# Kernel tuning notes

Measured on AMD Instinct MI355X. Metric: run time of the kernel, lower is better.

## Reference

```python
import jax, jax.numpy as jnp
import numpy as np

C = 128
NUM_GROUPS = 32
EPS = 1e-6


def setup_inputs() -> dict:
    key = jax.random.key(0)
    ks = jax.random.split(key, 6)
    B, H, W = 8, 64, 64
    x = jax.random.normal(ks[0], (B, C, H, W), dtype=jnp.float32)
    # 1x1 conv weights stored as [out_c, in_c] (kernel spatial dims are 1)
    fan_avg = C  # fan_in == fan_out == C for 1x1 conv
    bound = np.sqrt(3.0 / fan_avg)
    wq = jax.random.uniform(ks[1], (C, C), jnp.float32, -bound, bound)
    wk = jax.random.uniform(ks[2], (C, C), jnp.float32, -bound, bound)
    wv = jax.random.uniform(ks[3], (C, C), jnp.float32, -bound, bound)
    # proj_out has init_scale=0.0 -> near-zero init; use tiny random instead to test math
    wo = jax.random.uniform(ks[4], (C, C), jnp.float32, -bound, bound) * 1e-3
    bq = jnp.zeros((C,), jnp.float32)
    bk = jnp.zeros((C,), jnp.float32)
    bv = jnp.zeros((C,), jnp.float32)
    bo = jnp.zeros((C,), jnp.float32)
    gamma = jnp.ones((C,), jnp.float32)
    beta = jnp.zeros((C,), jnp.float32)
    return {"x": x, "gamma": gamma, "beta": beta,
            "wq": wq, "bq": bq, "wk": wk, "bk": bk,
            "wv": wv, "bv": bv, "wo": wo, "bo": bo}


def _group_norm(x, gamma, beta):
    B, Ch, H, W = x.shape
    g = NUM_GROUPS
    xg = x.reshape(B, g, Ch // g, H, W)
    mean = jnp.mean(xg, axis=(2, 3, 4), keepdims=True)
    var = jnp.var(xg, axis=(2, 3, 4), keepdims=True)
    xn = ((xg - mean) * jax.lax.rsqrt(var + EPS)).reshape(B, Ch, H, W)
    return xn * gamma[None, :, None, None] + beta[None, :, None, None]


def _conv1x1(x, w, b):
    # x: [B,C,H,W], w: [O,C], b: [O]
    return jnp.einsum('bchw,oc->bohw', x, w) + b[None, :, None, None]


def reference(x, gamma, beta, wq, bq, wk, bk, wv, bv, wo, bo):
    B, Ch, H, W = x.shape
    n = H * W
    h = _group_norm(x, gamma, beta)
    q = _conv1x1(h, wq, bq).reshape(B, Ch, n)
    k = _conv1x1(h, wk, bk).reshape(B, Ch, n)
    v = _conv1x1(h, wv, bv).reshape(B, Ch, n)
    # attn[b, i, j] = sum_c q[b,c,i] * k[b,c,j] / sqrt(C)
    attn = jnp.einsum('bci,bcj->bij', q, k) * (float(Ch) ** -0.5)
    attn = jax.nn.softmax(attn, axis=-1)
    # h[b,c,i] = sum_j v[b,c,j] * attn[b,i,j]
    out = jnp.einsum('bcj,bij->bci', v, attn).reshape(B, Ch, H, W)
    out = _conv1x1(out, wo, bo)
    return x + out
```

## Files before the change

### kernel.cpp

```cpp
#include <hip/hip_runtime.h>


typedef float f32x4 __attribute__((ext_vector_type(4)));
typedef short short8 __attribute__((ext_vector_type(8)));
typedef _Float16 half8 __attribute__((ext_vector_type(8)));
typedef _Float16 half2t __attribute__((ext_vector_type(2)));
typedef unsigned short ush;
typedef unsigned short ush4 __attribute__((ext_vector_type(4)));

__device__ __forceinline__ ush f2bf(float f) {
  unsigned u = __builtin_bit_cast(unsigned, f);
  u = (u + 0x7FFFu + ((u >> 16) & 1u)) >> 16;
  return (ush)u;
}
__device__ __forceinline__ float bf2f(ush v) {
  unsigned u = ((unsigned)v) << 16;
  return __builtin_bit_cast(float, u);
}
__device__ __forceinline__ unsigned f2fp8(float x) {
  unsigned u = __builtin_bit_cast(unsigned, x);
  unsigned s = (u >> 24) & 0x80u;
  unsigned au = u & 0x7fffffffu;
  if (au < 0x3A800000u) return s;
  if (au >= 0x43E00000u) return s | 0x7Eu;
  int e = (int)(au >> 23) - 127;
  if (e < -6) {
    float a = __builtin_bit_cast(float, au);
    int m = (int)(a * 512.0f + 0.5f);
    if (m >= 8) return s | 0x08u;
    return s | (unsigned)m;
  }
  unsigned keep = au >> 20, rem = au & 0xFFFFFu;
  keep += (rem > 0x80000u) || ((rem == 0x80000u) && (keep & 1u));
  int ef = (int)(keep >> 3) - 127;
  if (ef >= 8 && ((ef > 8) || ((keep & 7u) == 7u))) return s | 0x7Eu;
  return s | (unsigned)(((ef + 7) << 3) | (int)(keep & 7u));
}
__device__ __forceinline__ void async16(const void* g, void* l) {
  __builtin_amdgcn_global_load_lds(
      (const __attribute__((address_space(1))) unsigned int*)g,
      (__attribute__((address_space(3))) unsigned int*)l, 16, 0, 0);
}

__global__ __launch_bounds__(256) void gn_stats_kernel(
    const float* __restrict__ x, const float* __restrict__ gamma,
    const float* __restrict__ beta, const float* __restrict__ wo,
    float* __restrict__ scale_c, float* __restrict__ shift_c,
    ush* __restrict__ wob) {
  int bg = blockIdx.x;
  int b = bg >> 5, g = bg & 31;
  int tid = threadIdx.x;
  if (bg < 16) {
    int v4 = (bg * 256 + tid) * 4;
    float4 w4 = *(const float4*)(wo + v4);
    ush4 pk;
    pk.x = f2bf(w4.x); pk.y = f2bf(w4.y);
    pk.z = f2bf(w4.z); pk.w = f2bf(w4.w);
    *(ush4*)(wob + v4) = pk;
  }
  const float4* base = (const float4*)(x + (size_t)bg * 16384);
  float s = 0.f, sq = 0.f;
#pragma unroll
  for (int p = 0; p < 16; ++p) {
    float4 v = base[p * 256 + tid];
    s += (v.x + v.y) + (v.z + v.w);
    sq += (v.x * v.x + v.y * v.y) + (v.z * v.z + v.w * v.w);
  }
#pragma unroll
  for (int off = 32; off > 0; off >>= 1) {
    s += __shfl_down(s, off);
    sq += __shfl_down(sq, off);
  }
  __shared__ float rs[4], rq[4], mv[2];
  int w = tid >> 6, lane = tid & 63;
  if (lane == 0) { rs[w] = s; rq[w] = sq; }
  __syncthreads();
  if (tid == 0) {
    float S = (rs[0] + rs[1]) + (rs[2] + rs[3]);
    float Q = (rq[0] + rq[1]) + (rq[2] + rq[3]);
    float mean = S * (1.f / 16384.f);
    float var = Q * (1.f / 16384.f) - mean * mean;
    mv[0] = mean;
    mv[1] = rsqrtf(var + 1e-6f);
  }
  __syncthreads();
  if (tid < 4) {
    int c = (g << 2) + tid;
    float sc = mv[1] * gamma[c];
    scale_c[(b << 7) + c] = sc;
    shift_c[(b << 7) + c] = beta[c] - mv[0] * sc;
  }
}

__global__ __launch_bounds__(256) void qkv_kernel(
    const float* __restrict__ x, const float* __restrict__ scale_c,
    const float* __restrict__ shift_c, const float* __restrict__ wq,
    const float* __restrict__ wk, const float* __restrict__ wv,
    const float* __restrict__ bq, const float* __restrict__ bk,
    const float* __restrict__ bv, char* __restrict__ Qt8,
    char* __restrict__ Kt8, _Float16* __restrict__ Vh) {
  __shared__ __align__(16) ush hs[64 * 136];
  __shared__ __align__(16) ush wol[128 * 136];
  char* hs8 = (char*)hs;
  int bx = blockIdx.x;
  int type = bx >> 9;
  int rb = bx & 511;
  int b = rb >> 6, i0 = (rb & 63) << 6;
  int tid = threadIdx.x;
  int w = tid >> 6, lane = tid & 63, ln15 = lane & 15, quad = lane >> 4;

#pragma unroll
  for (int p = 0; p < 8; ++p) {
    int id = p * 256 + tid;
    int i = id & 63;
    int g8 = id >> 6;
    int c0 = g8 << 2;
    const float* xp = x + (((size_t)((b << 7) + c0)) << 12) + i0 + i;
    ush4 pk4;
#pragma unroll
    for (int e = 0; e < 4; ++e) {
      float h = xp[(size_t)e << 12] * scale_c[(b << 7) + c0 + e] +
                shift_c[(b << 7) + c0 + e];
      pk4[e] = f2bf(h);
    }
    int pg = g8 ^ ((i & 15) << 1);
    *(ush4*)(hs8 + i * 272 + pg * 8) = pk4;
  }
  const float* W = type == 0 ? wq : (type == 1 ? wk : wv);
#pragma unroll
  for (int p = 0; p < 16; ++p) {
    int v = p * 256 + tid;
    int o = v >> 5, cv = (v & 31) << 2;
    float4 w4 = *(const float4*)(W + (o << 7) + cv);
    uint2 pk;
    pk.x = (unsigned)f2bf(w4.x) | ((unsigned)f2bf(w4.y) << 16);
    pk.y = (unsigned)f2bf(w4.z) | ((unsigned)f2bf(w4.w) << 16);
    *(uint2*)&wol[o * 136 + cv] = pk;
  }
  __syncthreads();

#define HS_FRAG(row, dc) \
  (*(const short8*)(hs8 + (row) * 272 + (((((dc)*4 + quad)) ^ ((row)&15)) << 4)))

  if (type < 2) {
    f32x4 acc[8] = {};
    int hrow = w * 16 + ln15;
#pragma unroll
    for (int dc = 0; dc < 4; ++dc) {
      short8 af = HS_FRAG(hrow, dc);
#pragma unroll
      for (int nb = 0; nb < 8; ++nb) {
        short8 bf = *(const short8*)&wol[(nb * 16 + ln15) * 136 + dc * 32 + quad * 8];
        acc[nb] = __builtin_amdgcn_mfma_f32_16x16x32_bf16(af, bf, acc[nb], 0, 0, 0);
      }
    }
    const float* bias = type == 0 ? bq : bk;
    char* dst8 = type == 0 ? Qt8 : Kt8;
    __syncthreads();
#pragma unroll
    for (int nb = 0; nb < 8; ++nb) {
      int o = nb * 16 + ln15;
      float bi = bias[o];
#pragma unroll
      for (int r = 0; r < 4; ++r) {
        float val = acc[nb][r] + bi;
        if (type == 0) val *= 0.12751742f;
        hs8[(w * 16 + quad * 4 + r) * 144 + o] = (char)f2fp8(val);
      }
    }
    __syncthreads();
    int i = tid >> 2, seg = tid & 3;
    uint4 d0 = *(const uint4*)(hs8 + i * 144 + seg * 32);
    uint4 d1 = *(const uint4*)(hs8 + i * 144 + seg * 32 + 16);
    char* drow = dst8 + (((size_t)((b << 12) + i0 + i)) << 7) + seg * 32;
    *(uint4*)drow = d0;
    *(uint4*)(drow + 16) = d1;
  } else {
    f32x4 acc[8] = {};
    int hrow = w * 16 + ln15;
#pragma unroll
    for (int dc = 0; dc < 4; ++dc) {
      short8 bf = HS_FRAG(hrow, dc);
#pragma unroll
      for (int mb = 0; mb < 8; ++mb) {
        short8 af = *(const short8*)&wol[(mb * 16 + ln15) * 136 + dc * 32 + quad * 8];
        acc[mb] = __builtin_amdgcn_mfma_f32_16x16x32_bf16(af, bf, acc[mb], 0, 0, 0);
      }
    }
#pragma unroll
    for (int mb = 0; mb < 8; ++mb) {
#pragma unroll
      for (int r = 0; r < 4; ++r) {
        int o = mb * 16 + quad * 4 + r;
        float val = acc[mb][r] + bv[o];
        Vh[(((size_t)((b << 7) + o)) << 12) + i0 + w * 16 + ln15] = (_Float16)val;
      }
    }
  }
#undef HS_FRAG
}

__global__ __launch_bounds__(256, 3) void attn_kernel(
    const char* __restrict__ Qt8, const char* __restrict__ Kt8,
    const _Float16* __restrict__ Vh, ush* __restrict__ po,
    float* __restrict__ lw) {
  __shared__ __align__(16) char ksb[2][4096];
  __shared__ __align__(16) _Float16 vsb[2][4096];
  int bx = blockIdx.x;
  int b = bx & 7, qt = (bx >> 3) & 31, ksid = bx >> 8;
  int tid = threadIdx.x;
  int w = tid >> 6, lane = tid & 63, ln15 = lane & 15, quad = lane >> 4;
  int qbase = (qt << 7) + (w << 5);
  int j0 = ksid << 10;

  long qf[2][4];
#pragma unroll
  for (int ih = 0; ih < 2; ++ih) {
    const char* qrow =
        Qt8 + (((size_t)((b << 12) + qbase + ih * 16 + ln15)) << 7);
#pragma unroll
    for (int dc = 0; dc < 4; ++dc)
      qf[ih][dc] = *(const long*)(qrow + dc * 32 + quad * 8);
  }

  int kj = (w << 3) + (lane >> 3);
  int kh = (kj & 3) | (((kj >> 3) & 1) << 2);
  int kg = (lane & 7) ^ kh;
  const char* ksrc = Kt8 + (((size_t)((b << 12) + j0 + kj)) << 7) + (kg << 4);
  int d0r = (w << 5) + (lane >> 2);
  int d1r = d0r + 16;
  int vg0 = (lane & 3) ^ (((d0r >> 1) + (d0r >> 3)) & 3);
  int vg1 = (lane & 3) ^ (((d1r >> 1) + (d1r >> 3)) & 3);
  const _Float16* vsrc0 =
      Vh + (((size_t)((b << 7) + d0r)) << 12) + j0 + (vg0 << 3);
  const _Float16* vsrc1 =
      Vh + (((size_t)((b << 7) + d1r)) << 12) + j0 + (vg1 << 3);
  char* kdA = &ksb[0][0] + (w << 10);
  char* kdB = &ksb[1][0] + (w << 10);
  char* vdA0 = (char*)&vsb[0][0] + ((w * 2 + 0) << 10);
  char* vdA1 = (char*)&vsb[0][0] + ((w * 2 + 1) << 10);
  char* vdB0 = (char*)&vsb[1][0] + ((w * 2 + 0) << 10);
  char* vdB1 = (char*)&vsb[1][0] + ((w * 2 + 1) << 10);

  async16(ksrc, kdA);
  async16(vsrc0, vdA0);
  async16(vsrc1, vdA1);
  __syncthreads();

  f32x4 O[2][8] = {};
  float lsum[2] = {0.f, 0.f};
  const f32x4 SINIT = {-7.2134752f, -7.2134752f, -7.2134752f, -7.2134752f};
  int r0 = ((ln15 >> 2) << 3) + (ln15 & 3), r1 = r0 + 4;
  int hr = (ln15 & 3) | (((ln15 >> 2) & 1) << 2);

  for (int jt = 0; jt < 32; ++jt) {
    int buf = jt & 1;
    if (jt + 1 < 32) {
      ksrc += 4096;
      vsrc0 += 32;
      vsrc1 += 32;
      if (buf == 0) {
        async16(ksrc, kdB);
        async16(vsrc0, vdB0);
        async16(vsrc1, vdB1);
      } else {
        async16(ksrc, kdA);
        async16(vsrc0, vdA0);
        async16(vsrc1, vdA1);
      }
    }
    const char* kb = &ksb[buf][0];
    const char* vb = (const char*)&vsb[buf][0];

    f32x4 S[2][2];
#pragma unroll
    for (int ih = 0; ih < 2; ++ih) { S[ih][0] = SINIT; S[ih][1] = SINIT; }
#pragma unroll
    for (int dc = 0; dc < 4; ++dc) {
      int goff = ((((dc * 2 + (quad >> 1))) ^ hr) << 4) + ((quad & 1) << 3);
      long kf0 = *(const long*)(kb + r0 * 128 + goff);
      long kf1 = *(const long*)(kb + r1 * 128 + goff);
#pragma unroll
      for (int ih = 0; ih < 2; ++ih) {
        S[ih][0] = __builtin_amdgcn_mfma_f32_16x16x32_fp8_fp8(kf0, qf[ih][dc], S[ih][0], 0, 0, 0);
        S[ih][1] = __builtin_amdgcn_mfma_f32_16x16x32_fp8_fp8(kf1, qf[ih][dc], S[ih][1], 0, 0, 0);
      }
    }
    half8 pf[2];
#pragma unroll
    for (int ih = 0; ih < 2; ++ih) {
      float ls = 0.f;
      half8 p;
#pragma unroll
      for (int t = 0; t < 2; ++t) {
        float p0 = __builtin_amdgcn_exp2f(S[ih][t][0]);
        float p1 = __builtin_amdgcn_exp2f(S[ih][t][1]);
        float p2 = __builtin_amdgcn_exp2f(S[ih][t][2]);
        float p3 = __builtin_amdgcn_exp2f(S[ih][t][3]);
        ls += (p0 + p1) + (p2 + p3);
        half2t h01 = __builtin_bit_cast(half2t, __builtin_amdgcn_cvt_pkrtz(p0, p1));
        half2t h23 = __builtin_bit_cast(half2t, __builtin_amdgcn_cvt_pkrtz(p2, p3));
        p[t * 4 + 0] = h01.x; p[t * 4 + 1] = h01.y;
        p[t * 4 + 2] = h23.x; p[t * 4 + 3] = h23.y;
      }
      pf[ih] = p;
      lsum[ih] += ls;
    }
#pragma unroll
    for (int nb = 0; nb < 8; ++nb) {
      int d = nb * 16 + ln15;
      int sd = ((d >> 1) + (d >> 3)) & 3;
      half8 vf = *(const half8*)(vb + d * 64 + ((quad ^ sd) << 4));
#pragma unroll
      for (int ih = 0; ih < 2; ++ih)
        O[ih][nb] = __builtin_amdgcn_mfma_f32_16x16x32_f16(vf, pf[ih], O[ih][nb], 0, 0, 0);
    }
    __syncthreads();
  }

#pragma unroll
  for (int ih = 0; ih < 2; ++ih) {
    float l = lsum[ih];
    l += __shfl_xor(l, 16);
    l += __shfl_xor(l, 32);
    if (quad == 0) lw[(ksid << 15) + (b << 12) + qbase + ih * 16 + ln15] = l;
    int i = qbase + ih * 16 + ln15;
    size_t rowb = (((size_t)((ksid * 8 + b)) << 12) + i) << 7;
#pragma unroll
    for (int nb = 0; nb < 8; ++nb) {
      ush4 pk;
      pk.x = f2bf(O[ih][nb][0]);
      pk.y = f2bf(O[ih][nb][1]);
      pk.z = f2bf(O[ih][nb][2]);
      pk.w = f2bf(O[ih][nb][3]);
      *(ush4*)(po + rowb + nb * 16 + quad * 4) = pk;
    }
  }
}

__global__ __launch_bounds__(256) void proj_kernel(
    const float* __restrict__ x, const ush* __restrict__ po,
    const float* __restrict__ lw, const ush* __restrict__ wob,
    const float* __restrict__ bo, float* __restrict__ out) {
  int bx = blockIdx.x;
  int b = bx >> 6, i0 = (bx & 63) << 6;
  int tid = threadIdx.x;
  int w = tid >> 6, lane = tid & 63, ln15 = lane & 15, quad = lane >> 4;
  int i = i0 + w * 16 + ln15;
  float rl = 0.f;
#pragma unroll
  for (int s = 0; s < 4; ++s) rl += lw[(s << 15) + (b << 12) + i];
  float rinv = 1.f / rl;

  f32x4 acc[8] = {};
#pragma unroll
  for (int dc = 0; dc < 4; ++dc) {
    float vsum[8] = {0.f, 0.f, 0.f, 0.f, 0.f, 0.f, 0.f, 0.f};
#pragma unroll
    for (int s = 0; s < 4; ++s) {
      short8 pv = *(const short8*)(po + (((size_t)(s * 8 + b)) << 19) +
                                   ((size_t)i << 7) + dc * 32 + quad * 8);
#pragma unroll
      for (int e = 0; e < 8; ++e) vsum[e] += bf2f((ush)pv[e]);
    }
    short8 bfv;
#pragma unroll
    for (int e = 0; e < 8; ++e) bfv[e] = (short)f2bf(vsum[e] * rinv);
#pragma unroll
    for (int mb = 0; mb < 8; ++mb) {
      short8 af = *(const short8*)(wob + ((mb * 16 + ln15) << 7) + dc * 32 +
                                   quad * 8);
      acc[mb] = __builtin_amdgcn_mfma_f32_16x16x32_bf16(af, bfv, acc[mb], 0, 0, 0);
    }
  }
#pragma unroll
  for (int mb = 0; mb < 8; ++mb) {
#pragma unroll
    for (int r = 0; r < 4; ++r) {
      int o = mb * 16 + quad * 4 + r;
      size_t idx = (((size_t)(b << 7) + o) << 12) + i;
      out[idx] = x[idx] + acc[mb][r] + bo[o];
    }
  }
}

extern "C" void kernel_launch(void* const* d_in, const int* in_sizes, int n_in,
                              void* d_out, int out_size, void* d_ws,
                              size_t ws_size, hipStream_t stream) {
  const float* x = (const float*)d_in[0];
  const float* gamma = (const float*)d_in[1];
  const float* beta = (const float*)d_in[2];
  const float* wq = (const float*)d_in[3];
  const float* bq = (const float*)d_in[4];
  const float* wk = (const float*)d_in[5];
  const float* bk = (const float*)d_in[6];
  const float* wv = (const float*)d_in[7];
  const float* bv = (const float*)d_in[8];
  const float* wo = (const float*)d_in[9];
  const float* bo = (const float*)d_in[10];
  float* out = (float*)d_out;

  const size_t NE = (size_t)8 * 4096 * 128;
  char* Qt8 = (char*)d_ws;
  char* Kt8 = Qt8 + NE;
  _Float16* Vh = (_Float16*)(Kt8 + NE);
  ush* po = (ush*)(Vh + NE);
  float* lwp = (float*)(po + 4 * NE);
  float* scale_c = lwp + 4 * 32768;
  float* shift_c = scale_c + 1024;
  ush* wob = (ush*)(shift_c + 1024);

  gn_stats_kernel<<<256, 256, 0, stream>>>(x, gamma, beta, wo, scale_c,
                                           shift_c, wob);
  qkv_kernel<<<1536, 256, 0, stream>>>(x, scale_c, shift_c, wq, wk, wv, bq, bk,
                                       bv, Qt8, Kt8, Vh);
  attn_kernel<<<1024, 256, 0, stream>>>(Qt8, Kt8, Vh, po, lwp);
  proj_kernel<<<512, 256, 0, stream>>>(x, po, lwp, wob, bo, out);
}
```

Before: 200.0 us.

## Software-pipeline QK^T one tile ahead of softmax and PV in attention loop

Restructures the attention inner loop so the QK^T scores for tile jt+1 are computed while the exp/PV work for tile jt proceeds. K is now prefetched two tiles ahead and V one tile ahead in separate double buffers. Matrix phases are wrapped in s_setprio to raise wave priority during MFMA issue. The goal is to hide exp latency and LDS load latency behind matrix work, at the cost of more live registers (an extra score array) and an extra barrier in the prologue.

```diff
diff --git a/kernel.cpp b/kernel.cpp
--- a/kernel.cpp
+++ b/kernel.cpp
@@ -245,6 +245,8 @@
   async16(ksrc, kdA);
   async16(vsrc0, vdA0);
   async16(vsrc1, vdA1);
+  ksrc += 4096;
+  async16(ksrc, kdB);
   __syncthreads();
 
   f32x4 O[2][8] = {};
@@ -253,28 +255,11 @@
   int r0 = ((ln15 >> 2) << 3) + (ln15 & 3), r1 = r0 + 4;
   int hr = (ln15 & 3) | (((ln15 >> 2) & 1) << 2);
 
-  for (int jt = 0; jt < 32; ++jt) {
-    int buf = jt & 1;
-    if (jt + 1 < 32) {
-      ksrc += 4096;
-      vsrc0 += 32;
-      vsrc1 += 32;
-      if (buf == 0) {
-        async16(ksrc, kdB);
-        async16(vsrc0, vdB0);
-        async16(vsrc1, vdB1);
-      } else {
-        async16(ksrc, kdA);
-        async16(vsrc0, vdA0);
-        async16(vsrc1, vdA1);
-      }
-    }
-    const char* kb = &ksb[buf][0];
-    const char* vb = (const char*)&vsb[buf][0];
-
-    f32x4 S[2][2];
-#pragma unroll
-    for (int ih = 0; ih < 2; ++ih) { S[ih][0] = SINIT; S[ih][1] = SINIT; }
+  f32x4 Sc[2][2];
+#pragma unroll
+  for (int ih = 0; ih < 2; ++ih) { Sc[ih][0] = SINIT; Sc[ih][1] = SINIT; }
+  {
+    const char* kb = &ksb[0][0];
 #pragma unroll
     for (int dc = 0; dc < 4; ++dc) {
       int goff = ((((dc * 2 + (quad >> 1))) ^ hr) << 4) + ((quad & 1) << 3);
@@ -282,10 +267,51 @@
       long kf1 = *(const long*)(kb + r1 * 128 + goff);
 #pragma unroll
       for (int ih = 0; ih < 2; ++ih) {
-        S[ih][0] = __builtin_amdgcn_mfma_f32_16x16x32_fp8_fp8(kf0, qf[ih][dc], S[ih][0], 0, 0, 0);
-        S[ih][1] = __builtin_amdgcn_mfma_f32_16x16x32_fp8_fp8(kf1, qf[ih][dc], S[ih][1], 0, 0, 0);
-      }
-    }
+        Sc[ih][0] = __builtin_amdgcn_mfma_f32_16x16x32_fp8_fp8(kf0, qf[ih][dc], Sc[ih][0], 0, 0, 0);
+        Sc[ih][1] = __builtin_amdgcn_mfma_f32_16x16x32_fp8_fp8(kf1, qf[ih][dc], Sc[ih][1], 0, 0, 0);
+      }
+    }
+  }
+  __syncthreads();
+
+  for (int jt = 0; jt < 32; ++jt) {
+    if (jt + 2 < 32) {
+      ksrc += 4096;
+      async16(ksrc, (jt & 1) ? kdB : kdA);
+    }
+    if (jt + 1 < 32) {
+      vsrc0 += 32;
+      vsrc1 += 32;
+      if (jt & 1) {
+        async16(vsrc0, vdA0);
+        async16(vsrc1, vdA1);
+      } else {
+        async16(vsrc0, vdB0);
+        async16(vsrc1, vdB1);
+      }
+    }
+    const char* kbn = (jt & 1) ? &ksb[0][0] : &ksb[1][0];
+    const char* vb = (const char*)((jt & 1) ? &vsb[1][0] : &vsb[0][0]);
+
+    f32x4 Sn[2][2];
+    if (jt + 1 < 32) {
+#pragma unroll
+      for (int ih = 0; ih < 2; ++ih) { Sn[ih][0] = SINIT; Sn[ih][1] = SINIT; }
+      __builtin_amdgcn_s_setprio(1);
+#pragma unroll
+      for (int dc = 0; dc < 4; ++dc) {
+        int goff = ((((dc * 2 + (quad >> 1))) ^ hr) << 4) + ((quad & 1) << 3);
+        long kf0 = *(const long*)(kbn + r0 * 128 + goff);
+        long kf1 = *(const long*)(kbn + r1 * 128 + goff);
+#pragma unroll
+        for (int ih = 0; ih < 2; ++ih) {
+          Sn[ih][0] = __builtin_amdgcn_mfma_f32_16x16x32_fp8_fp8(kf0, qf[ih][dc], Sn[ih][0], 0, 0, 0);
+          Sn[ih][1] = __builtin_amdgcn_mfma_f32_16x16x32_fp8_fp8(kf1, qf[ih][dc], Sn[ih][1], 0, 0, 0);
+        }
+      }
+      __builtin_amdgcn_s_setprio(0);
+    }
+
     half8 pf[2];
 #pragma unroll
     for (int ih = 0; ih < 2; ++ih) {
@@ -293,10 +319,10 @@
       half8 p;
 #pragma unroll
       for (int t = 0; t < 2; ++t) {
-        float p0 = __builtin_amdgcn_exp2f(S[ih][t][0]);
-        float p1 = __builtin_amdgcn_exp2f(S[ih][t][1]);
-        float p2 = __builtin_amdgcn_exp2f(S[ih][t][2]);
-        float p3 = __builtin_amdgcn_exp2f(S[ih][t][3]);
+        float p0 = __builtin_amdgcn_exp2f(Sc[ih][t][0]);
+        float p1 = __builtin_amdgcn_exp2f(Sc[ih][t][1]);
+        float p2 = __builtin_amdgcn_exp2f(Sc[ih][t][2]);
+        float p3 = __builtin_amdgcn_exp2f(Sc[ih][t][3]);
         ls += (p0 + p1) + (p2 + p3);
         half2t h01 = __builtin_bit_cast(half2t, __builtin_amdgcn_cvt_pkrtz(p0, p1));
         half2t h23 = __builtin_bit_cast(half2t, __builtin_amdgcn_cvt_pkrtz(p2, p3));
@@ -306,6 +332,8 @@
       pf[ih] = p;
       lsum[ih] += ls;
     }
+
+    __builtin_amdgcn_s_setprio(1);
 #pragma unroll
     for (int nb = 0; nb < 8; ++nb) {
       int d = nb * 16 + ln15;
@@ -315,7 +343,16 @@
       for (int ih = 0; ih < 2; ++ih)
         O[ih][nb] = __builtin_amdgcn_mfma_f32_16x16x32_f16(vf, pf[ih], O[ih][nb], 0, 0, 0);
     }
+    __builtin_amdgcn_s_setprio(0);
     __syncthreads();
+
+    if (jt + 1 < 32) {
+#pragma unroll
+      for (int ih = 0; ih < 2; ++ih) {
+        Sc[ih][0] = Sn[ih][0];
+        Sc[ih][1] = Sn[ih][1];
+      }
+    }
   }
 
 #pragma unroll
```

Result: no change. 199.4 us (-0.3%).

## Use 4-stage LDS ring with prefetch distance two and explicit vmcnt waits

Applied to the files above, without the earlier changes.

The attention kernel's K/V shared-memory staging changes from a double buffer to a four-slot ring. Loads are issued two tiles ahead, and each iteration waits on vmcnt with a single barrier instead of the trailing __syncthreads. It also raises wave priority around the MFMA blocks with s_setprio. This should hide global-to-LDS latency better, but it doubles LDS use (48KB per block), which may limit occupancy under launch_bounds(256,3).

```diff
diff --git a/kernel.cpp b/kernel.cpp
--- a/kernel.cpp
+++ b/kernel.cpp
@@ -204,8 +204,8 @@
     const char* __restrict__ Qt8, const char* __restrict__ Kt8,
     const _Float16* __restrict__ Vh, ush* __restrict__ po,
     float* __restrict__ lw) {
-  __shared__ __align__(16) char ksb[2][4096];
-  __shared__ __align__(16) _Float16 vsb[2][4096];
+  __shared__ __align__(16) char ksb[4][4096];
+  __shared__ __align__(16) _Float16 vsb[4][4096];
   int bx = blockIdx.x;
   int b = bx & 7, qt = (bx >> 3) & 31, ksid = bx >> 8;
   int tid = threadIdx.x;
@@ -235,17 +235,18 @@
       Vh + (((size_t)((b << 7) + d0r)) << 12) + j0 + (vg0 << 3);
   const _Float16* vsrc1 =
       Vh + (((size_t)((b << 7) + d1r)) << 12) + j0 + (vg1 << 3);
-  char* kdA = &ksb[0][0] + (w << 10);
-  char* kdB = &ksb[1][0] + (w << 10);
-  char* vdA0 = (char*)&vsb[0][0] + ((w * 2 + 0) << 10);
-  char* vdA1 = (char*)&vsb[0][0] + ((w * 2 + 1) << 10);
-  char* vdB0 = (char*)&vsb[1][0] + ((w * 2 + 0) << 10);
-  char* vdB1 = (char*)&vsb[1][0] + ((w * 2 + 1) << 10);
-
-  async16(ksrc, kdA);
-  async16(vsrc0, vdA0);
-  async16(vsrc1, vdA1);
-  __syncthreads();
+
+  asm volatile("s_waitcnt vmcnt(0)" ::: "memory");
+
+  async16(ksrc, &ksb[0][0] + (w << 10));
+  async16(vsrc0, (char*)&vsb[0][0] + ((2 * w + 0) << 10));
+  async16(vsrc1, (char*)&vsb[0][0] + ((2 * w + 1) << 10));
+  ksrc += 4096;
+  vsrc0 += 32;
+  vsrc1 += 32;
+  async16(ksrc, &ksb[1][0] + (w << 10));
+  async16(vsrc0, (char*)&vsb[1][0] + ((2 * w + 0) << 10));
+  async16(vsrc1, (char*)&vsb[1][0] + ((2 * w + 1) << 10));
 
   f32x4 O[2][8] = {};
   float lsum[2] = {0.f, 0.f};
@@ -254,27 +255,28 @@
   int hr = (ln15 & 3) | (((ln15 >> 2) & 1) << 2);
 
   for (int jt = 0; jt < 32; ++jt) {
-    int buf = jt & 1;
-    if (jt + 1 < 32) {
+    if (jt < 31)
+      asm volatile("s_waitcnt vmcnt(3)" ::: "memory");
+    else
+      asm volatile("s_waitcnt vmcnt(0)" ::: "memory");
+    __builtin_amdgcn_s_barrier();
+
+    if (jt + 2 < 32) {
       ksrc += 4096;
       vsrc0 += 32;
       vsrc1 += 32;
-      if (buf == 0) {
-        async16(ksrc, kdB);
-        async16(vsrc0, vdB0);
-        async16(vsrc1, vdB1);
-      } else {
-        async16(ksrc, kdA);
-        async16(vsrc0, vdA0);
-        async16(vsrc1, vdA1);
-      }
-    }
-    const char* kb = &ksb[buf][0];
-    const char* vb = (const char*)&vsb[buf][0];
+      int rd = (jt + 2) & 3;
+      async16(ksrc, &ksb[rd][0] + (w << 10));
+      async16(vsrc0, (char*)&vsb[rd][0] + ((2 * w + 0) << 10));
+      async16(vsrc1, (char*)&vsb[rd][0] + ((2 * w + 1) << 10));
+    }
+    const char* kb = &ksb[jt & 3][0];
+    const char* vb = (const char*)&vsb[jt & 3][0];
 
     f32x4 S[2][2];
 #pragma unroll
     for (int ih = 0; ih < 2; ++ih) { S[ih][0] = SINIT; S[ih][1] = SINIT; }
+    __builtin_amdgcn_s_setprio(1);
 #pragma unroll
     for (int dc = 0; dc < 4; ++dc) {
       int goff = ((((dc * 2 + (quad >> 1))) ^ hr) << 4) + ((quad & 1) << 3);
@@ -286,6 +288,8 @@
         S[ih][1] = __builtin_amdgcn_mfma_f32_16x16x32_fp8_fp8(kf1, qf[ih][dc], S[ih][1], 0, 0, 0);
       }
     }
+    __builtin_amdgcn_s_setprio(0);
+
     half8 pf[2];
 #pragma unroll
     for (int ih = 0; ih < 2; ++ih) {
@@ -306,6 +310,8 @@
       pf[ih] = p;
       lsum[ih] += ls;
     }
+
+    __builtin_amdgcn_s_setprio(1);
 #pragma unroll
     for (int nb = 0; nb < 8; ++nb) {
       int d = nb * 16 + ln15;
@@ -315,7 +321,7 @@
       for (int ih = 0; ih < 2; ++ih)
         O[ih][nb] = __builtin_amdgcn_mfma_f32_16x16x32_f16(vf, pf[ih], O[ih][nb], 0, 0, 0);
     }
-    __syncthreads();
+    __builtin_amdgcn_s_setprio(0);
   }
 
 #pragma unroll
```

Result: slower. 208.7 us (+4.3%).

## Interleave QK score and softmax per row-half, add setprio, raise occupancy

Applied to the files above, without the earlier changes.

The attention inner loop now computes the QK scores for one 16-row half and immediately applies exp2 and fp16 packing before moving to the next half. This cuts the live score registers from four accumulators to two. Launch bounds rise from 3 to 4 blocks per CU so the freed registers can buy occupancy, and s_setprio is raised around the MFMA sections to favour matrix issue over other waves. Risks are register spills under the tighter bound, a different MFMA/exp overlap pattern, and K fragments being loaded twice from LDS, once per half.

```diff
diff --git a/kernel.cpp b/kernel.cpp
--- a/kernel.cpp
+++ b/kernel.cpp
@@ -7,6 +7,7 @@
 typedef _Float16 half2t __attribute__((ext_vector_type(2)));
 typedef unsigned short ush;
 typedef unsigned short ush4 __attribute__((ext_vector_type(4)));
+typedef unsigned int uint4t __attribute__((ext_vector_type(4)));
 
 __device__ __forceinline__ ush f2bf(float f) {
   unsigned u = __builtin_bit_cast(unsigned, f);
@@ -200,7 +201,7 @@
 #undef HS_FRAG
 }
 
-__global__ __launch_bounds__(256, 3) void attn_kernel(
+__global__ __launch_bounds__(256, 4) void attn_kernel(
     const char* __restrict__ Qt8, const char* __restrict__ Kt8,
     const _Float16* __restrict__ Vh, ush* __restrict__ po,
     float* __restrict__ lw) {
@@ -272,40 +273,45 @@
     const char* kb = &ksb[buf][0];
     const char* vb = (const char*)&vsb[buf][0];
 
-    f32x4 S[2][2];
-#pragma unroll
-    for (int ih = 0; ih < 2; ++ih) { S[ih][0] = SINIT; S[ih][1] = SINIT; }
-#pragma unroll
-    for (int dc = 0; dc < 4; ++dc) {
-      int goff = ((((dc * 2 + (quad >> 1))) ^ hr) << 4) + ((quad & 1) << 3);
-      long kf0 = *(const long*)(kb + r0 * 128 + goff);
-      long kf1 = *(const long*)(kb + r1 * 128 + goff);
-#pragma unroll
-      for (int ih = 0; ih < 2; ++ih) {
-        S[ih][0] = __builtin_amdgcn_mfma_f32_16x16x32_fp8_fp8(kf0, qf[ih][dc], S[ih][0], 0, 0, 0);
-        S[ih][1] = __builtin_amdgcn_mfma_f32_16x16x32_fp8_fp8(kf1, qf[ih][dc], S[ih][1], 0, 0, 0);
-      }
-    }
     half8 pf[2];
 #pragma unroll
     for (int ih = 0; ih < 2; ++ih) {
-      float ls = 0.f;
-      half8 p;
-#pragma unroll
-      for (int t = 0; t < 2; ++t) {
-        float p0 = __builtin_amdgcn_exp2f(S[ih][t][0]);
-        float p1 = __builtin_amdgcn_exp2f(S[ih][t][1]);
-        float p2 = __builtin_amdgcn_exp2f(S[ih][t][2]);
-        float p3 = __builtin_amdgcn_exp2f(S[ih][t][3]);
-        ls += (p0 + p1) + (p2 + p3);
-        half2t h01 = __builtin_bit_cast(half2t, __builtin_amdgcn_cvt_pkrtz(p0, p1));
-        half2t h23 = __builtin_bit_cast(half2t, __builtin_amdgcn_cvt_pkrtz(p2, p3));
-        p[t * 4 + 0] = h01.x; p[t * 4 + 1] = h01.y;
-        p[t * 4 + 2] = h23.x; p[t * 4 + 3] = h23.y;
-      }
-      pf[ih] = p;
-      lsum[ih] += ls;
-    }
+      f32x4 s0, s1;
+      __builtin_amdgcn_s_setprio(1);
+      {
+        int goff = (((quad >> 1) ^ hr) << 4) + ((quad & 1) << 3);
+        long kf0 = *(const long*)(kb + r0 * 128 + goff);
+        long kf1 = *(const long*)(kb + r1 * 128 + goff);
+        s0 = __builtin_amdgcn_mfma_f32_16x16x32_fp8_fp8(kf0, qf[ih][0], SINIT, 0, 0, 0);
+        s1 = __builtin_amdgcn_mfma_f32_16x16x32_fp8_fp8(kf1, qf[ih][0], SINIT, 0, 0, 0);
+      }
+#pragma unroll
+      for (int dc = 1; dc < 4; ++dc) {
+        int goff = ((((dc * 2 + (quad >> 1))) ^ hr) << 4) + ((quad & 1) << 3);
+        long kf0 = *(const long*)(kb + r0 * 128 + goff);
+        long kf1 = *(const long*)(kb + r1 * 128 + goff);
+        s0 = __builtin_amdgcn_mfma_f32_16x16x32_fp8_fp8(kf0, qf[ih][dc], s0, 0, 0, 0);
+        s1 = __builtin_amdgcn_mfma_f32_16x16x32_fp8_fp8(kf1, qf[ih][dc], s1, 0, 0, 0);
+      }
+      __builtin_amdgcn_s_setprio(0);
+      float p0 = __builtin_amdgcn_exp2f(s0[0]);
+      float p1 = __builtin_amdgcn_exp2f(s0[1]);
+      float p2 = __builtin_amdgcn_exp2f(s0[2]);
+      float p3 = __builtin_amdgcn_exp2f(s0[3]);
+      float p4 = __builtin_amdgcn_exp2f(s1[0]);
+      float p5 = __builtin_amdgcn_exp2f(s1[1]);
+      float p6 = __builtin_amdgcn_exp2f(s1[2]);
+      float p7 = __builtin_amdgcn_exp2f(s1[3]);
+      lsum[ih] += ((p0 + p1) + (p2 + p3)) + ((p4 + p5) + (p6 + p7));
+      uint4t pw;
+      pw.x = __builtin_bit_cast(unsigned, __builtin_amdgcn_cvt_pkrtz(p0, p1));
+      pw.y = __builtin_bit_cast(unsigned, __builtin_amdgcn_cvt_pkrtz(p2, p3));
+      pw.z = __builtin_bit_cast(unsigned, __builtin_amdgcn_cvt_pkrtz(p4, p5));
+      pw.w = __builtin_bit_cast(unsigned, __builtin_amdgcn_cvt_pkrtz(p6, p7));
+      pf[ih] = __builtin_bit_cast(half8, pw);
+    }
+
+    __builtin_amdgcn_s_setprio(1);
 #pragma unroll
     for (int nb = 0; nb < 8; ++nb) {
       int d = nb * 16 + ln15;
@@ -315,6 +321,7 @@
       for (int ih = 0; ih < 2; ++ih)
         O[ih][nb] = __builtin_amdgcn_mfma_f32_16x16x32_f16(vf, pf[ih], O[ih][nb], 0, 0, 0);
     }
+    __builtin_amdgcn_s_setprio(0);
     __syncthreads();
   }
 
```

Measured after the change: 214.4 us. 1.07x slower.
